# Kernel tuning notes

Hardware: AMD Instinct MI355X
Metric: run time of the kernel (lower is better)

## Reference

```python
import jax, jax.numpy as jnp
import numpy as np
import math

EARTH_RADIUS_KM = 6371.0
D_MAX_KM = 200.0
K_D = 64

B, N, D, R = 64, 128, 128, 4096


def setup_inputs() -> dict:
    key = jax.random.key(0)
    ks = jax.random.split(key, 7)
    S = jax.random.normal(ks[0], (B, N, D), dtype=jnp.float32)
    region_emb = jax.random.normal(ks[1], (R, D), dtype=jnp.float32)
    traj_lat = jax.random.uniform(ks[2], (B, N), dtype=jnp.float32)
    traj_lon = jax.random.uniform(ks[3], (B, N), dtype=jnp.float32)
    region_centroids = jax.random.uniform(ks[4], (R, 2), dtype=jnp.float32)
    key_padding_mask = jax.random.randint(ks[5], (B, N), 0, 2).astype(bool)
    E_d_match = jax.random.normal(ks[6], (K_D,), dtype=jnp.float32) * 0.1
    return {"S": S, "region_emb": region_emb, "traj_lat": traj_lat,
            "traj_lon": traj_lon, "region_centroids": region_centroids,
            "key_padding_mask": key_padding_mask, "E_d_match": E_d_match}


def _haversine_km(lat1, lon1, lat2, lon2):
    deg2rad = math.pi / 180.0
    lat1r = lat1 * deg2rad
    lat2r = lat2 * deg2rad
    dlat = (lat2 - lat1) * deg2rad
    dlon = (lon2 - lon1) * deg2rad
    a = jnp.sin(dlat / 2) ** 2 + jnp.cos(lat1r) * jnp.cos(lat2r) * jnp.sin(dlon / 2) ** 2
    a = jnp.clip(a, 0.0, 1.0)
    return EARTH_RADIUS_KM * 2.0 * jnp.arcsin(jnp.sqrt(a))


def _interp_scalar(table, x):
    K = table.shape[0]
    x = jnp.clip(x, 0.0, K - 1 - 1e-06)
    k = jnp.floor(x).astype(jnp.int32)
    frac = x - k.astype(x.dtype)
    lo = table[k]
    hi = table[jnp.minimum(k + 1, K - 1)]
    return (1.0 - frac) * lo + frac * hi


def reference(S, region_emb, traj_lat, traj_lon, region_centroids,
              key_padding_mask, E_d_match):
    Dm = S.shape[-1]
    cand_lat = region_centroids[:, 0]  # [R]
    cand_lon = region_centroids[:, 1]
    # [B, n, R] pairwise distance trajectory-position <-> region centroid
    dd = _haversine_km(traj_lat[:, :, None], traj_lon[:, :, None],
                       cand_lat[None, None, :], cand_lon[None, None, :])
    d_bin = jnp.clip(dd, 0.0, D_MAX_KM) / D_MAX_KM * (K_D - 1)
    bias_match = _interp_scalar(E_d_match, d_bin)  # [B, n, R]
    scores = jnp.einsum('bnd,rd->bnr', S, region_emb) / math.sqrt(Dm)
    scores = scores + bias_match
    mask = key_padding_mask[:, :, None]  # [B, n, 1]
    scores = jnp.where(mask, -jnp.inf, scores)
    attn = jnp.nan_to_num(jax.nn.softmax(scores, axis=1), nan=0.0)
    scores_safe = jnp.where(mask, 0.0, scores)
    return (attn * scores_safe).sum(axis=1)  # [B, R]
```

## Files before the change

kernel.cpp:

```cpp
#include <hip/hip_runtime.h>
#include <math.h>

#define BB 64
#define NN 128
#define DD 128
#define RR 4096
#define KD 64

typedef _Float16 f16x8 __attribute__((ext_vector_type(8)));
typedef _Float16 f16x4 __attribute__((ext_vector_type(4)));
typedef float    float4v __attribute__((ext_vector_type(4)));

#define WS_E_OFF   0
#define WS_S_OFF   (1048576)
#define WS_CG_OFF  (3145728)
#define WS_RG_OFF  (3145728 + 65536)
#define WS_TAB_OFF (3145728 + 65536 + 131072)
#define WS_V_OFF   (3145728 + 65536 + 131072 + 512)

#define D2R_C    0.017453292519943295f
#define HSC_C    (0.008726646259971648f * 4013.73f)
#define L2E_C    1.4426950408889634f
#define SCALE2_C (0.08838834764831845f * 1.4426950408889634f)
#define LN2_C    0.6931471805599453f

__global__ __launch_bounds__(256)
void prep_kernel(const float* __restrict__ S, const float* __restrict__ E,
                 const float* __restrict__ tlat, const float* __restrict__ tlon,
                 const float* __restrict__ cent, const int* __restrict__ kpm,
                 const float* __restrict__ Etab, char* __restrict__ wsb) {
    const int blk = blockIdx.x, tid = threadIdx.x;
    if (blk < 512) {
        int i = blk * 256 + tid;
        float4 v = ((const float4*)E)[i];
        f16x4 h = {(_Float16)v.x, (_Float16)v.y, (_Float16)v.z, (_Float16)v.w};
        ((f16x4*)(wsb + WS_E_OFF))[i] = h;
    } else if (blk < 528) {
        int r = (blk - 512) * 256 + tid;
        float cla = cent[2 * r], clo = cent[2 * r + 1];
        ((float4*)(wsb + WS_CG_OFF))[r] =
            make_float4(cla * HSC_C, clo * HSC_C, cosf(cla * D2R_C), 0.0f);
    } else if (blk == 528) {
        if (tid < KD) {
            float lo = Etab[tid];
            float hi = Etab[tid < KD - 1 ? tid + 1 : KD - 1];
            ((float2*)(wsb + WS_TAB_OFF))[tid] =
                make_float2(lo * L2E_C, (hi - lo) * L2E_C);
        }
    } else {
        __shared__ int idx[128];
        __shared__ unsigned long long smask[2];
        const int b = blk - 529;
        const int wv = tid >> 6, lane = tid & 63;
        if (tid < 128) {
            bool valid = (kpm[b * NN + tid] == 0);
            unsigned long long m = __ballot(valid);
            if (lane == 0) smask[wv] = m;
        }
        __syncthreads();
        const unsigned long long m0 = smask[0], m1 = smask[1];
        const int c0 = __popcll(m0);
        const int V  = c0 + __popcll(m1);
        if (tid == 0) ((int*)(wsb + WS_V_OFF))[b] = V;
        if (tid < 128) {
            unsigned long long mw = (tid < 64) ? m0 : m1;
            int ln = tid & 63;
            if ((mw >> ln) & 1ull) {
                int pos = __popcll(mw & ((1ull << ln) - 1ull)) + (tid < 64 ? 0 : c0);
                idx[pos] = tid;
            }
        }
        __syncthreads();
        if (tid < 128) {
            float4 rg;
            if (tid < V) {
                int n = idx[tid];
                float la = tlat[b * NN + n], lo = tlon[b * NN + n];
                rg = make_float4(la * HSC_C, lo * HSC_C, cosf(la * D2R_C), 0.0f);
            } else rg = make_float4(0.0f, 0.0f, -1.0f, 0.0f);
            ((float4*)(wsb + WS_RG_OFF))[b * 128 + tid] = rg;
        }
        f16x4* dst = (f16x4*)(wsb + WS_S_OFF) + (size_t)b * NN * (DD / 4);
        const float4* src = (const float4*)S + (size_t)b * NN * (DD / 4);
        for (int ch = tid; ch < V * 32; ch += 256) {
            int row = ch >> 5, cp = ch & 31;
            float4 v = src[idx[row] * 32 + cp];
            f16x4 h = {(_Float16)v.x, (_Float16)v.y, (_Float16)v.z, (_Float16)v.w};
            dst[row * 32 + cp] = h;
        }
    }
}

__global__ __launch_bounds__(256, 4)
void matching_kernel(const char* __restrict__ wsb, float* __restrict__ out) {
    __shared__ _Float16 ldsE[64 * 128];
    __shared__ float colLatX[64], colLonX[64], colCos[64];
    __shared__ float rowLatX[128], rowLonX[128], rowCn[128];
    __shared__ float2 tab2[KD];
    __shared__ float pe[4][64], pw[4][64];

    const int tid = threadIdx.x;
    const int b  = blockIdx.y;
    const int r0 = blockIdx.x * 64;
    const int wv = tid >> 6, lane = tid & 63;
    const int lrow = lane & 15, quad = lane >> 4;

    const _Float16* wsE = (const _Float16*)(wsb + WS_E_OFF);
    const _Float16* wsS = (const _Float16*)(wsb + WS_S_OFF);

    const int V  = ((const int*)(wsb + WS_V_OFF))[b];

    uint4 creg[4];
    int srowv[4], scv[4];
#pragma unroll
    for (int t = 0; t < 4; ++t) {
        int i = tid + t * 256;
        srowv[t] = i >> 4; scv[t] = i & 15;
        creg[t] = *(const uint4*)(wsE + (size_t)(r0 + srowv[t]) * DD + scv[t] * 8);
    }
    float4 cg, rg; float2 t2;
    if (tid < 64)        cg = ((const float4*)(wsb + WS_CG_OFF))[r0 + tid];
    else if (tid < 128)  t2 = ((const float2*)(wsb + WS_TAB_OFF))[tid - 64];
    else                 rg = ((const float4*)(wsb + WS_RG_OFF))[b * 128 + (tid - 128)];

    const _Float16* pA0 = wsS + (size_t)(b * NN + wv * 16 + lrow) * DD;
    f16x8 af0[4];
#pragma unroll
    for (int kk = 0; kk < 4; ++kk)
        af0[kk] = *(const f16x8*)(pA0 + kk * 32 + quad * 8);

    const int Mt = (V + 15) >> 4;
    const bool t1a = (wv + 4) < Mt;

#pragma unroll
    for (int t = 0; t < 4; ++t)
        *(uint4*)&ldsE[srowv[t] * DD + ((scv[t] ^ (srowv[t] & 7)) * 8)] = creg[t];
    if (tid < 64) { colLatX[tid] = cg.x; colLonX[tid] = cg.y; colCos[tid] = cg.z; }
    else if (tid < 128) tab2[tid - 64] = t2;
    else { int n = tid - 128; rowLatX[n] = rg.x; rowLonX[n] = rg.y; rowCn[n] = rg.z; }
    __syncthreads();

    float4v acc[2][4] = {};
#pragma unroll
    for (int kk = 0; kk < 4; ++kk) {
#pragma unroll
        for (int tr = 0; tr < 4; ++tr) {
            int row = tr * 16 + lrow;
            int c = kk * 4 + quad;
            f16x8 bb = *(const f16x8*)&ldsE[row * DD + ((c ^ (lrow & 7)) * 8)];
            acc[0][tr] = __builtin_amdgcn_mfma_f32_16x16x32_f16(af0[kk], bb, acc[0][tr], 0, 0, 0);
        }
    }
    if (t1a) {
        const _Float16* pA1 = pA0 + 64 * DD;
        f16x8 af1[4];
#pragma unroll
        for (int kk = 0; kk < 4; ++kk)
            af1[kk] = *(const f16x8*)(pA1 + kk * 32 + quad * 8);
#pragma unroll
        for (int kk = 0; kk < 4; ++kk) {
#pragma unroll
            for (int tr = 0; tr < 4; ++tr) {
                int row = tr * 16 + lrow;
                int c = kk * 4 + quad;
                f16x8 bb = *(const f16x8*)&ldsE[row * DD + ((c ^ (lrow & 7)) * 8)];
                acc[1][tr] = __builtin_amdgcn_mfma_f32_16x16x32_f16(af1[kk], bb, acc[1][tr], 0, 0, 0);
            }
        }
    }

    float tlX[8], toX[8], cn8[8];
#pragma unroll
    for (int i = 0; i < 2; ++i)
#pragma unroll
        for (int e = 0; e < 4; ++e) {
            int n = (wv + 4 * i) * 16 + quad * 4 + e;
            int j = i * 4 + e;
            tlX[j] = rowLatX[n]; toX[j] = rowLonX[n]; cn8[j] = rowCn[n];
        }

#pragma unroll
    for (int tr = 0; tr < 4; ++tr) {
        int col = tr * 16 + lrow;
        float claX = colLatX[col], cloX = colLonX[col], cc = colCos[col];
        float es = 0.0f, ws2 = 0.0f;
#pragma unroll
        for (int i = 0; i < 2; ++i) {
            if (i == 1 && !t1a) continue;
#pragma unroll
            for (int e = 0; e < 4; ++e) {
                int j = i * 4 + e;
                float hd = claX - tlX[j];
                float ho = cloX - toX[j];
                float a  = fmaf(hd, hd, (cn8[j] * cc) * (ho * ho));
                float x  = fminf(__builtin_amdgcn_sqrtf(a), 62.999996f);
                int   k  = (int)x;
                float fr = x - (float)k;
                float2 te = tab2[k];
                float bias2 = fmaf(fr, te.y, te.x);
                float s2 = fmaf(acc[i][tr][e], SCALE2_C, bias2);
                float ex = __builtin_amdgcn_exp2f(s2);
                ex = (cn8[j] < 0.0f) ? 0.0f : ex;
                es += ex;
                ws2 = fmaf(ex, s2, ws2);
            }
        }
        es  += __shfl_xor(es, 16, 64);  es  += __shfl_xor(es, 32, 64);
        ws2 += __shfl_xor(ws2, 16, 64); ws2 += __shfl_xor(ws2, 32, 64);
        if (lane < 16) { pe[wv][col] = es; pw[wv][col] = ws2; }
    }
    __syncthreads();

    if (tid < 64) {
        float es = pe[0][tid] + pe[1][tid] + pe[2][tid] + pe[3][tid];
        float ws = pw[0][tid] + pw[1][tid] + pw[2][tid] + pw[3][tid];
        float o = es > 0.0f ? (ws / es) * LN2_C : 0.0f;
        out[(size_t)b * RR + r0 + tid] = o;
    }
}

extern "C" void kernel_launch(void* const* d_in, const int* in_sizes, int n_in,
                              void* d_out, int out_size, void* d_ws, size_t ws_size,
                              hipStream_t stream) {
    const float* S    = (const float*)d_in[0];
    const float* Remb = (const float*)d_in[1];
    const float* tlat = (const float*)d_in[2];
    const float* tlon = (const float*)d_in[3];
    const float* cent = (const float*)d_in[4];
    const int*   kpm  = (const int*)d_in[5];
    const float* Etab = (const float*)d_in[6];
    float* out = (float*)d_out;
    char* wsb = (char*)d_ws;

    prep_kernel<<<593, 256, 0, stream>>>(S, Remb, tlat, tlon, cent, kpm, Etab, wsb);

    dim3 grid(RR / 64, BB, 1);
    matching_kernel<<<grid, dim3(256, 1, 1), 0, stream>>>(wsb, out);
}
```

Baseline: 94.73 us.

## Process four region tiles per block with double-buffered LDS prefetch

Each block now handles 256 regions in four 64-region tiles. The next tile's embeddings and centroids are prefetched into registers while the current tile computes, and are staged through a double-buffered LDS array. The S fragments and row geometry are loaded once per block and reused across the four tiles, which cuts redundant global loads and per-block setup. In exchange the grid shrinks from 4096 to 1024 blocks, so there is less parallelism and less latency hiding across blocks, and LDS and register use per block go up.

After: 116.0 us. +22.5%, slower.

```diff
diff --git a/kernel.cpp b/kernel.cpp
--- a/kernel.cpp
+++ b/kernel.cpp
@@ -93,15 +93,15 @@
 
 __global__ __launch_bounds__(256, 4)
 void matching_kernel(const char* __restrict__ wsb, float* __restrict__ out) {
-    __shared__ _Float16 ldsE[64 * 128];
-    __shared__ float colLatX[64], colLonX[64], colCos[64];
+    __shared__ _Float16 ldsE[2][64 * 128];
+    __shared__ float colL[2][64], colO[2][64], colC[2][64];
     __shared__ float rowLatX[128], rowLonX[128], rowCn[128];
     __shared__ float2 tab2[KD];
     __shared__ float pe[4][64], pw[4][64];
 
     const int tid = threadIdx.x;
-    const int b  = blockIdx.y;
-    const int r0 = blockIdx.x * 64;
+    const int b     = blockIdx.y;
+    const int rbase = blockIdx.x * 256;
     const int wv = tid >> 6, lane = tid & 63;
     const int lrow = lane & 15, quad = lane >> 4;
 
@@ -110,112 +110,113 @@
 
     const int V  = ((const int*)(wsb + WS_V_OFF))[b];
 
+    float4 rg; float2 t2;
+    if (tid >= 128)     rg = ((const float4*)(wsb + WS_RG_OFF))[b * 128 + (tid - 128)];
+    else if (tid >= 64) t2 = ((const float2*)(wsb + WS_TAB_OFF))[tid - 64];
+
+    const _Float16* pA0 = wsS + (size_t)(b * NN + wv * 16 + lrow) * DD;
+    f16x8 af0[4], af1[4];
+#pragma unroll
+    for (int kk = 0; kk < 4; ++kk) {
+        af0[kk] = *(const f16x8*)(pA0 + kk * 32 + quad * 8);
+        af1[kk] = *(const f16x8*)(pA0 + 64 * DD + kk * 32 + quad * 8);
+    }
+
+    const int srow0 = tid >> 4, scc = tid & 15;
     uint4 creg[4];
-    int srowv[4], scv[4];
-#pragma unroll
+#pragma unroll
+    for (int tc = 0; tc < 4; ++tc)
+        creg[tc] = *(const uint4*)(wsE + (size_t)(rbase + srow0 + tc * 16) * DD + scc * 8);
+    float4 cg;
+    if (tid < 64) cg = ((const float4*)(wsb + WS_CG_OFF))[rbase + tid];
+
+    if (tid >= 128) { int n = tid - 128; rowLatX[n] = rg.x; rowLonX[n] = rg.y; rowCn[n] = rg.z; }
+    else if (tid >= 64) tab2[tid - 64] = t2;
+
+    const int Mt  = (V + 15) >> 4;
+    const bool t1a = (wv + 4) < Mt;
+
+    float tlX[8], toX[8], cn8[8];
+
     for (int t = 0; t < 4; ++t) {
-        int i = tid + t * 256;
-        srowv[t] = i >> 4; scv[t] = i & 15;
-        creg[t] = *(const uint4*)(wsE + (size_t)(r0 + srowv[t]) * DD + scv[t] * 8);
-    }
-    float4 cg, rg; float2 t2;
-    if (tid < 64)        cg = ((const float4*)(wsb + WS_CG_OFF))[r0 + tid];
-    else if (tid < 128)  t2 = ((const float2*)(wsb + WS_TAB_OFF))[tid - 64];
-    else                 rg = ((const float4*)(wsb + WS_RG_OFF))[b * 128 + (tid - 128)];
-
-    const _Float16* pA0 = wsS + (size_t)(b * NN + wv * 16 + lrow) * DD;
-    f16x8 af0[4];
-#pragma unroll
-    for (int kk = 0; kk < 4; ++kk)
-        af0[kk] = *(const f16x8*)(pA0 + kk * 32 + quad * 8);
-
-    const int Mt = (V + 15) >> 4;
-    const bool t1a = (wv + 4) < Mt;
-
-#pragma unroll
-    for (int t = 0; t < 4; ++t)
-        *(uint4*)&ldsE[srowv[t] * DD + ((scv[t] ^ (srowv[t] & 7)) * 8)] = creg[t];
-    if (tid < 64) { colLatX[tid] = cg.x; colLonX[tid] = cg.y; colCos[tid] = cg.z; }
-    else if (tid < 128) tab2[tid - 64] = t2;
-    else { int n = tid - 128; rowLatX[n] = rg.x; rowLonX[n] = rg.y; rowCn[n] = rg.z; }
-    __syncthreads();
-
-    float4v acc[2][4] = {};
-#pragma unroll
-    for (int kk = 0; kk < 4; ++kk) {
-#pragma unroll
-        for (int tr = 0; tr < 4; ++tr) {
-            int row = tr * 16 + lrow;
-            int c = kk * 4 + quad;
-            f16x8 bb = *(const f16x8*)&ldsE[row * DD + ((c ^ (lrow & 7)) * 8)];
-            acc[0][tr] = __builtin_amdgcn_mfma_f32_16x16x32_f16(af0[kk], bb, acc[0][tr], 0, 0, 0);
-        }
-    }
-    if (t1a) {
-        const _Float16* pA1 = pA0 + 64 * DD;
-        f16x8 af1[4];
-#pragma unroll
-        for (int kk = 0; kk < 4; ++kk)
-            af1[kk] = *(const f16x8*)(pA1 + kk * 32 + quad * 8);
+        const int p = t & 1;
+#pragma unroll
+        for (int tc = 0; tc < 4; ++tc) {
+            int sr = srow0 + tc * 16;
+            *(uint4*)&ldsE[p][sr * 128 + ((scc ^ (sr & 7)) * 8)] = creg[tc];
+        }
+        if (tid < 64) { colL[p][tid] = cg.x; colO[p][tid] = cg.y; colC[p][tid] = cg.z; }
+        if (t < 3) {
+#pragma unroll
+            for (int tc = 0; tc < 4; ++tc)
+                creg[tc] = *(const uint4*)(wsE + (size_t)(rbase + (t + 1) * 64 + srow0 + tc * 16) * DD + scc * 8);
+            if (tid < 64) cg = ((const float4*)(wsb + WS_CG_OFF))[rbase + (t + 1) * 64 + tid];
+        }
+        __syncthreads();
+
+        if (t == 0) {
+#pragma unroll
+            for (int i = 0; i < 2; ++i)
+#pragma unroll
+                for (int e = 0; e < 4; ++e) {
+                    int n = (wv + 4 * i) * 16 + quad * 4 + e;
+                    int j = i * 4 + e;
+                    tlX[j] = rowLatX[n]; toX[j] = rowLonX[n]; cn8[j] = rowCn[n];
+                }
+        }
+
+        float4v acc[2][4] = {};
 #pragma unroll
         for (int kk = 0; kk < 4; ++kk) {
 #pragma unroll
             for (int tr = 0; tr < 4; ++tr) {
                 int row = tr * 16 + lrow;
                 int c = kk * 4 + quad;
-                f16x8 bb = *(const f16x8*)&ldsE[row * DD + ((c ^ (lrow & 7)) * 8)];
-                acc[1][tr] = __builtin_amdgcn_mfma_f32_16x16x32_f16(af1[kk], bb, acc[1][tr], 0, 0, 0);
+                f16x8 bb = *(const f16x8*)&ldsE[p][row * 128 + ((c ^ (lrow & 7)) * 8)];
+                acc[0][tr] = __builtin_amdgcn_mfma_f32_16x16x32_f16(af0[kk], bb, acc[0][tr], 0, 0, 0);
+                if (t1a)
+                    acc[1][tr] = __builtin_amdgcn_mfma_f32_16x16x32_f16(af1[kk], bb, acc[1][tr], 0, 0, 0);
             }
         }
-    }
-
-    float tlX[8], toX[8], cn8[8];
-#pragma unroll
-    for (int i = 0; i < 2; ++i)
-#pragma unroll
-        for (int e = 0; e < 4; ++e) {
-            int n = (wv + 4 * i) * 16 + quad * 4 + e;
-            int j = i * 4 + e;
-            tlX[j] = rowLatX[n]; toX[j] = rowLonX[n]; cn8[j] = rowCn[n];
-        }
-
-#pragma unroll
-    for (int tr = 0; tr < 4; ++tr) {
-        int col = tr * 16 + lrow;
-        float claX = colLatX[col], cloX = colLonX[col], cc = colCos[col];
-        float es = 0.0f, ws2 = 0.0f;
-#pragma unroll
-        for (int i = 0; i < 2; ++i) {
-            if (i == 1 && !t1a) continue;
-#pragma unroll
-            for (int e = 0; e < 4; ++e) {
-                int j = i * 4 + e;
-                float hd = claX - tlX[j];
-                float ho = cloX - toX[j];
-                float a  = fmaf(hd, hd, (cn8[j] * cc) * (ho * ho));
-                float x  = fminf(__builtin_amdgcn_sqrtf(a), 62.999996f);
-                int   k  = (int)x;
-                float fr = x - (float)k;
-                float2 te = tab2[k];
-                float bias2 = fmaf(fr, te.y, te.x);
-                float s2 = fmaf(acc[i][tr][e], SCALE2_C, bias2);
-                float ex = __builtin_amdgcn_exp2f(s2);
-                ex = (cn8[j] < 0.0f) ? 0.0f : ex;
-                es += ex;
-                ws2 = fmaf(ex, s2, ws2);
+
+#pragma unroll
+        for (int tr = 0; tr < 4; ++tr) {
+            int col = tr * 16 + lrow;
+            float claX = colL[p][col], cloX = colO[p][col], cc = colC[p][col];
+            float es = 0.0f, ws2 = 0.0f;
+#pragma unroll
+            for (int i = 0; i < 2; ++i) {
+                if (i == 1 && !t1a) continue;
+#pragma unroll
+                for (int e = 0; e < 4; ++e) {
+                    int j = i * 4 + e;
+                    float hd = claX - tlX[j];
+                    float ho = cloX - toX[j];
+                    float a  = fmaf(hd, hd, (cn8[j] * cc) * (ho * ho));
+                    float x  = fminf(__builtin_amdgcn_sqrtf(a), 62.999996f);
+                    int   k  = (int)x;
+                    float fr = x - (float)k;
+                    float2 te = tab2[k];
+                    float bias2 = fmaf(fr, te.y, te.x);
+                    float s2 = fmaf(acc[i][tr][e], SCALE2_C, bias2);
+                    float ex = __builtin_amdgcn_exp2f(s2);
+                    ex = (cn8[j] < 0.0f) ? 0.0f : ex;
+                    es += ex;
+                    ws2 = fmaf(ex, s2, ws2);
+                }
             }
-        }
-        es  += __shfl_xor(es, 16, 64);  es  += __shfl_xor(es, 32, 64);
-        ws2 += __shfl_xor(ws2, 16, 64); ws2 += __shfl_xor(ws2, 32, 64);
-        if (lane < 16) { pe[wv][col] = es; pw[wv][col] = ws2; }
-    }
-    __syncthreads();
-
-    if (tid < 64) {
-        float es = pe[0][tid] + pe[1][tid] + pe[2][tid] + pe[3][tid];
-        float ws = pw[0][tid] + pw[1][tid] + pw[2][tid] + pw[3][tid];
-        float o = es > 0.0f ? (ws / es) * LN2_C : 0.0f;
-        out[(size_t)b * RR + r0 + tid] = o;
+            es  += __shfl_xor(es, 16, 64);  es  += __shfl_xor(es, 32, 64);
+            ws2 += __shfl_xor(ws2, 16, 64); ws2 += __shfl_xor(ws2, 32, 64);
+            if (lane < 16) { pe[wv][col] = es; pw[wv][col] = ws2; }
+        }
+        __syncthreads();
+
+        if (tid < 64) {
+            float es = pe[0][tid] + pe[1][tid] + pe[2][tid] + pe[3][tid];
+            float ws = pw[0][tid] + pw[1][tid] + pw[2][tid] + pw[3][tid];
+            float o = es > 0.0f ? (ws / es) * LN2_C : 0.0f;
+            out[(size_t)b * RR + rbase + t * 64 + tid] = o;
+        }
     }
 }
 
@@ -234,6 +235,6 @@
 
     prep_kernel<<<593, 256, 0, stream>>>(S, Remb, tlat, tlon, cent, kpm, Etab, wsb);
 
-    dim3 grid(RR / 64, BB, 1);
+    dim3 grid(16, BB, 1);
     matching_kernel<<<grid, dim3(256, 1, 1), 0, stream>>>(wsb, out);
 }
```
